# Kernel optimization log

Hardware: AMD Instinct MI355X
Metric: run time of the kernel (lower is better)

## Reference

```python
import jax, jax.numpy as jnp
import numpy as np
from jax import lax

SCORE_THRESHOLD = 0.02
IOU_THRESHOLD = 0.5
NUM_CLASSES = 80
MAX_DETECTIONS = 10  # tf.image.non_max_suppression max_output_size in the source
ANCHORS = np.array([[1.08, 1.19], [3.42, 4.41], [6.63, 11.38], [9.42, 5.11], [16.62, 10.52]], dtype=np.float32)


def setup_inputs() -> dict:
    key = jax.random.key(0)
    k1, _ = jax.random.split(key)
    B, H, W = 16, 76, 76
    A = ANCHORS.shape[0]
    feats = jax.random.normal(k1, (B, H, W, A * (5 + NUM_CLASSES)), dtype=jnp.float32)
    anchors = jnp.asarray(ANCHORS)
    return {"feats": feats, "anchors": anchors}


def yolo_head(feats, anchors, num_classes):
    """Standard YOLOv2 decode (interpret_prediction)."""
    B, H, W, _ = feats.shape
    A = anchors.shape[0]
    feats = feats.reshape(B, H, W, A, 5 + num_classes)
    gy, gx = jnp.meshgrid(jnp.arange(H), jnp.arange(W), indexing="ij")
    grid = jnp.stack([gx, gy], axis=-1).astype(feats.dtype)  # [H,W,2] in (x,y) order
    conv_dims = jnp.array([W, H], dtype=feats.dtype)
    box_xy = (jax.nn.sigmoid(feats[..., 0:2]) + grid[None, :, :, None, :]) / conv_dims
    box_wh = jnp.exp(feats[..., 2:4]) * anchors[None, None, None, :, :] / conv_dims
    box_confidence = jax.nn.sigmoid(feats[..., 4:5])
    box_class_probs = jax.nn.softmax(feats[..., 5:], axis=-1)
    return box_xy, box_wh, box_confidence, box_class_probs


def _postprocess(feats, anchors):
    box_xy, box_wh, box_confidence, box_class_probs = yolo_head(feats, anchors, NUM_CLASSES)
    box_mins = box_xy - box_wh / 2.0
    box_maxes = box_xy + box_wh / 2.0
    # [y_min, x_min, y_max, x_max] as in the source (indices 1 then 0)
    boxes = jnp.concatenate([box_mins[..., 1:2], box_mins[..., 0:1], box_maxes[..., 1:2], box_maxes[..., 0:1]], axis=-1)
    box_scores = box_confidence * box_class_probs           # [B,H,W,A,C]
    box_classes = jnp.argmax(box_scores, axis=-1)           # [B,H,W,A]
    box_class_scores = jnp.max(box_scores, axis=-1)         # [B,H,W,A]

    # tf.boolean_mask flattens across all dims; emulate with fixed shapes by
    # marking below-threshold candidates as invalid (score -1).
    flat_boxes = boxes.reshape(-1, 4)                       # [N,4]
    flat_scores = box_class_scores.reshape(-1)              # [N]
    flat_classes = box_classes.reshape(-1)                  # [N]
    scores_work = jnp.where(flat_scores >= SCORE_THRESHOLD, flat_scores, -1.0)

    N = flat_boxes.shape[0]
    areas = jnp.maximum(flat_boxes[:, 2] - flat_boxes[:, 0], 0.0) * jnp.maximum(flat_boxes[:, 3] - flat_boxes[:, 1], 0.0)
    idx_range = jnp.arange(N)

    def step(sw, _):
        idx = jnp.argmax(sw)
        s = sw[idx]
        valid = s >= SCORE_THRESHOLD
        box = flat_boxes[idx]                               # [4] = y1,x1,y2,x2
        iy1 = jnp.maximum(box[0], flat_boxes[:, 0])
        ix1 = jnp.maximum(box[1], flat_boxes[:, 1])
        iy2 = jnp.minimum(box[2], flat_boxes[:, 2])
        ix2 = jnp.minimum(box[3], flat_boxes[:, 3])
        inter = jnp.maximum(iy2 - iy1, 0.0) * jnp.maximum(ix2 - ix1, 0.0)
        box_area = jnp.maximum(box[2] - box[0], 0.0) * jnp.maximum(box[3] - box[1], 0.0)
        iou = inter / (box_area + areas - inter + 1e-9)
        suppress = (iou > IOU_THRESHOLD) | (idx_range == idx)
        sw_new = jnp.where(valid & suppress, -1.0, sw)
        row = jnp.concatenate([box, s[None], flat_classes[idx].astype(jnp.float32)[None]])  # [6]
        row = jnp.where(valid, row, jnp.zeros_like(row))
        return sw_new, row

    _, rows = lax.scan(step, scores_work, None, length=MAX_DETECTIONS)
    return rows  # [MAX_DETECTIONS, 6] = [y1,x1,y2,x2,score,class]; zero rows are padding


def reference(feats, anchors):
    return _postprocess(feats, anchors)
```

## Files before the change

### kernel.cpp

```cpp
#include <hip/hip_runtime.h>
#include <stdint.h>

#define N_CAND 462080
#define NBINS  8192
#define HIST_BLOCKS 64
#define TARGET 256u
#define SMAX   1024
#define SCORE_THR 0.02f


typedef const __attribute__((address_space(1))) uint32_t* gas1_u32;
typedef __attribute__((address_space(3))) uint32_t*       las3_u32;
#define GLOAD_LDS16(g, l) __builtin_amdgcn_global_load_lds( \
    (gas1_u32)(const void*)(g), (las3_u32)(void*)(l), 16, 0, 0)

__global__ __launch_bounds__(64) void decode_kernel(
    const float* __restrict__ feats,
    float* __restrict__ scores, unsigned char* __restrict__ cls)
{
    __shared__ __align__(16) float lds[64 * 85];
    const int t = threadIdx.x;
    const long long base = (long long)blockIdx.x * 64;

    const float4* __restrict__ src = (const float4*)(feats + base * 85);
    float4* dst = (float4*)lds;
#pragma unroll
    for (int i = 0; i < 21; ++i)
        GLOAD_LDS16(src + i * 64 + t, dst + i * 64 + t);
    if (t < 16) GLOAD_LDS16(src + 21 * 64 + t, dst + 21 * 64 + t);

    asm volatile("s_waitcnt vmcnt(0)" ::: "memory");
    __builtin_amdgcn_sched_barrier(0);

    const float* f = lds + t * 85;
    const int ci = (int)base + t;

    float m = f[5];
    int cbest = 0;
#pragma unroll
    for (int k = 1; k < 80; ++k) {
        float v = f[5 + k];
        if (v > m) { m = v; cbest = k; }
    }
    float s0 = 0.f, s1 = 0.f, s2 = 0.f, s3 = 0.f;
#pragma unroll
    for (int k = 0; k < 80; k += 4) {
        s0 += __expf(f[5 + k] - m);
        s1 += __expf(f[6 + k] - m);
        s2 += __expf(f[7 + k] - m);
        s3 += __expf(f[8 + k] - m);
    }
    float ssum = (s0 + s1) + (s2 + s3);
    float conf = 1.0f / (1.0f + __expf(-f[4]));
    float score = conf * (1.0f / ssum);

    cls[ci] = (unsigned char)cbest;
    scores[ci] = (score >= SCORE_THR) ? score : -1.0f;
}

__global__ __launch_bounds__(1024) void hist_kernel(
    const float* __restrict__ scores, unsigned short* __restrict__ hist_part)
{
    __shared__ unsigned int lh[NBINS];
    const int t = threadIdx.x;
#pragma unroll
    for (int i = 0; i < 8; ++i) lh[t * 8 + i] = 0u;
    __syncthreads();

    for (int i = blockIdx.x * 1024 + t; i < N_CAND; i += HIST_BLOCKS * 1024) {
        float s = scores[i];
        if (s >= SCORE_THR) {
            int bin = (int)(s * (float)NBINS);
            bin = bin > (NBINS - 1) ? (NBINS - 1) : bin;
            atomicAdd(&lh[bin], 1u);
        }
    }
    __syncthreads();
    unsigned short* outp = hist_part + (size_t)blockIdx.x * NBINS;
#pragma unroll
    for (int i = 0; i < 8; ++i)
        outp[t * 8 + i] = (unsigned short)lh[t * 8 + i];
}

__global__ __launch_bounds__(1024) void cutoff_kernel(
    const unsigned short* __restrict__ hist_part, unsigned int* __restrict__ ctrl)
{
    __shared__ unsigned int lh[NBINS];
    __shared__ unsigned int pa[1024], pb[1024];
    const int t = threadIdx.x;

    unsigned bsum[8];
#pragma unroll
    for (int i = 0; i < 8; ++i) bsum[i] = 0u;
    for (int p = 0; p < HIST_BLOCKS; ++p) {
        const unsigned short* hp = hist_part + (size_t)p * NBINS + t * 8;
#pragma unroll
        for (int i = 0; i < 8; ++i) bsum[i] += hp[i];
    }
    unsigned s = 0;
#pragma unroll
    for (int i = 0; i < 8; ++i) { lh[t * 8 + i] = bsum[i]; s += bsum[i]; }
    pa[t] = s;
    __syncthreads();

    unsigned int* srcb = pa; unsigned int* dstb = pb;
    for (int off = 1; off < 1024; off <<= 1) {
        unsigned v = srcb[t] + ((t + off < 1024) ? srcb[t + off] : 0u);
        dstb[t] = v;
        __syncthreads();
        unsigned int* tmp = srcb; srcb = dstb; dstb = tmp;
    }
    unsigned St = srcb[t];
    unsigned Sn = (t < 1023) ? srcb[t + 1] : 0u;

    if (t == 0) {
        ctrl[0] = 0u;
        if (St < TARGET) ctrl[1] = 0u;
    }
    if (St >= TARGET && Sn < TARGET) {
        unsigned run = Sn;
#pragma unroll
        for (int i = 7; i >= 0; --i) {
            run += lh[t * 8 + i];
            if (run >= TARGET) { ctrl[1] = (unsigned)(t * 8 + i); break; }
        }
    }
}

__global__ __launch_bounds__(256) void compact_kernel(
    const float* __restrict__ scores, unsigned int* __restrict__ ctrl,
    float* __restrict__ lscore, int* __restrict__ lidx)
{
    int i = blockIdx.x * 256 + threadIdx.x;
    float sw = scores[i];
    if (sw >= SCORE_THR) {
        int bin = (int)(sw * (float)NBINS);
        bin = bin > (NBINS - 1) ? (NBINS - 1) : bin;
        if (bin >= (int)ctrl[1]) {
            unsigned pos = atomicAdd(&ctrl[0], 1u);
            if (pos < SMAX) { lscore[pos] = sw; lidx[pos] = i; }
        }
    }
}

__device__ inline float4 decode_box(const float* __restrict__ feats,
                                    const float* __restrict__ anchors, int ci)
{
    int a = ci % 5;
    int cell = ci / 5;
    int gx = cell % 76;
    int gy = (cell / 76) % 76;
    const float* f = feats + (long long)ci * 85;
    float bx = (1.0f / (1.0f + __expf(-f[0])) + (float)gx) / 76.0f;
    float by = (1.0f / (1.0f + __expf(-f[1])) + (float)gy) / 76.0f;
    float bw = __expf(f[2]) * anchors[2 * a]     / 76.0f;
    float bh = __expf(f[3]) * anchors[2 * a + 1] / 76.0f;
    return make_float4(by - bh * 0.5f, bx - bw * 0.5f,
                       by + bh * 0.5f, bx + bw * 0.5f);
}

__global__ __launch_bounds__(1024) void nms_kernel(
    const float* __restrict__ lscore, const int* __restrict__ lidx,
    const unsigned int* __restrict__ ctrl,
    const float* __restrict__ feats, const float* __restrict__ anchors,
    const unsigned char* __restrict__ cls, float* __restrict__ out)
{
    __shared__ unsigned long long wkey[16];
    __shared__ unsigned long long bkey;
    __shared__ float4 bbox;
    const int t = threadIdx.x;

    unsigned cnt = ctrl[0];
    int n = (cnt < (unsigned)SMAX) ? (int)cnt : SMAX;

    unsigned long long key = 0ull;
    float4 mb = make_float4(0.f, 0.f, 0.f, 0.f);
    float  msc = 0.f, mcls = 0.f;
    unsigned midx = 0xFFFFFFFFu;
    bool aliveb = false;
    if (t < n) {
        msc  = lscore[t];
        midx = (unsigned)lidx[t];
        key  = ((unsigned long long)__float_as_uint(msc) << 32)
             | (unsigned long long)(0xFFFFFFFFu - midx);
        mb   = decode_box(feats, anchors, (int)midx);
        mcls = (float)cls[midx];
        aliveb = true;
    }

    for (int r = 0; r < 10; ++r) {
        unsigned long long k0 = aliveb ? key : 0ull;
#pragma unroll
        for (int msk = 32; msk > 0; msk >>= 1) {
            unsigned long long o = __shfl_xor(k0, msk);
            k0 = (o > k0) ? o : k0;
        }
        if ((t & 63) == 0) wkey[t >> 6] = k0;
        __syncthreads();
        if (t < 16) {
            unsigned long long v = wkey[t];
#pragma unroll
            for (int msk = 8; msk > 0; msk >>= 1) {
                unsigned long long o = __shfl_xor(v, msk);
                v = (o > v) ? o : v;
            }
            if (t == 0) bkey = v;
        }
        __syncthreads();

        unsigned long long wk = bkey;
        bool have = (wk != 0ull);
        unsigned widx = 0xFFFFFFFFu;
        if (have) widx = 0xFFFFFFFFu - (unsigned)(wk & 0xFFFFFFFFull);

        if (have && aliveb && midx == widx) {
            bbox = mb;
            out[r * 6 + 0] = mb.x;
            out[r * 6 + 1] = mb.y;
            out[r * 6 + 2] = mb.z;
            out[r * 6 + 3] = mb.w;
            out[r * 6 + 4] = msc;
            out[r * 6 + 5] = mcls;
            aliveb = false;
        }
        if (!have && t == 0) {
#pragma unroll
            for (int q = 0; q < 6; ++q) out[r * 6 + q] = 0.f;
        }
        __syncthreads();

        if (have && aliveb) {
            float4 ab = bbox;
            float aarea = fmaxf(ab.z - ab.x, 0.f) * fmaxf(ab.w - ab.y, 0.f);
            float iy1 = fmaxf(ab.x, mb.x);
            float ix1 = fmaxf(ab.y, mb.y);
            float iy2 = fminf(ab.z, mb.z);
            float ix2 = fminf(ab.w, mb.w);
            float inter = fmaxf(iy2 - iy1, 0.f) * fmaxf(ix2 - ix1, 0.f);
            float carea = fmaxf(mb.z - mb.x, 0.f) * fmaxf(mb.w - mb.y, 0.f);
            float iou = inter / (aarea + carea - inter + 1e-9f);
            if (iou > 0.5f) aliveb = false;
        }
    }
}

extern "C" void kernel_launch(void* const* d_in, const int* in_sizes, int n_in,
                              void* d_out, int out_size, void* d_ws, size_t ws_size,
                              hipStream_t stream) {
    const float* feats   = (const float*)d_in[0];
    const float* anchors = (const float*)d_in[1];
    char* ws = (char*)d_ws;

    unsigned int*   ctrl      = (unsigned int*)(ws + 0);
    unsigned short* hist_part = (unsigned short*)(ws + 256);
    float*          lscore    = (float*)(ws + 1048832);
    int*            lidx      = (int*)(ws + 1052928);
    float*          scores    = (float*)(ws + 1057024);
    unsigned char*  cls       = (unsigned char*)(ws + 2905344);
    float*          out       = (float*)d_out;

    decode_kernel <<<N_CAND / 64, 64, 0, stream>>>(feats, scores, cls);
    hist_kernel   <<<HIST_BLOCKS, 1024, 0, stream>>>(scores, hist_part);
    cutoff_kernel <<<1, 1024, 0, stream>>>(hist_part, ctrl);
    compact_kernel<<<N_CAND / 256, 256, 0, stream>>>(scores, ctrl, lscore, lidx);
    nms_kernel    <<<1, 1024, 0, stream>>>(lscore, lidx, ctrl, feats, anchors, cls, out);
}
```

Measured before the change: 65.25 us.

## Fuse cutoff into histogram and NMS into compaction via last-block counters

Merges the single-block cutoff kernel into the histogram kernel and the single-block NMS kernel into the compaction kernel. In each fused kernel, the last block to finish, found with an atomic counter and thread fences, runs the serial stage. The counters are reset inside the decode kernel. This removes two kernel launches and their gaps, and halves the number of histogram partials, at the cost of relying on fence ordering and a tail stage that runs serially in one block.

Measured after the change: 182.0 us. +178.9%, slower.

```diff
diff --git a/kernel.cpp b/kernel.cpp
--- a/kernel.cpp
+++ b/kernel.cpp
@@ -3,10 +3,12 @@
 
 #define N_CAND 462080
 #define NBINS  8192
-#define HIST_BLOCKS 64
+#define HIST_BLOCKS 32
 #define TARGET 256u
 #define SMAX   1024
 #define SCORE_THR 0.02f
+#define CPB 1024
+#define COMPACT_BLOCKS ((N_CAND + CPB - 1) / CPB)
 
 
 typedef const __attribute__((address_space(1))) uint32_t* gas1_u32;
@@ -16,11 +18,14 @@
 
 __global__ __launch_bounds__(64) void decode_kernel(
     const float* __restrict__ feats,
-    float* __restrict__ scores, unsigned char* __restrict__ cls)
+    float* __restrict__ scores, unsigned char* __restrict__ cls,
+    unsigned int* __restrict__ ctrl)
 {
     __shared__ __align__(16) float lds[64 * 85];
     const int t = threadIdx.x;
     const long long base = (long long)blockIdx.x * 64;
+
+    if (blockIdx.x == 0 && t == 0) { ctrl[2] = 0u; ctrl[3] = 0u; }
 
     const float4* __restrict__ src = (const float4*)(feats + base * 85);
     float4* dst = (float4*)lds;
@@ -58,11 +63,15 @@
     scores[ci] = (score >= SCORE_THR) ? score : -1.0f;
 }
 
-__global__ __launch_bounds__(1024) void hist_kernel(
-    const float* __restrict__ scores, unsigned short* __restrict__ hist_part)
+__global__ __launch_bounds__(1024) void hist_cutoff_kernel(
+    const float* __restrict__ scores, unsigned short* __restrict__ hist_part,
+    unsigned int* __restrict__ ctrl)
 {
     __shared__ unsigned int lh[NBINS];
+    __shared__ unsigned int pa[1024], pb[1024];
+    __shared__ int lastf;
     const int t = threadIdx.x;
+
 #pragma unroll
     for (int i = 0; i < 8; ++i) lh[t * 8 + i] = 0u;
     __syncthreads();
@@ -80,14 +89,15 @@
 #pragma unroll
     for (int i = 0; i < 8; ++i)
         outp[t * 8 + i] = (unsigned short)lh[t * 8 + i];
-}
-
-__global__ __launch_bounds__(1024) void cutoff_kernel(
-    const unsigned short* __restrict__ hist_part, unsigned int* __restrict__ ctrl)
-{
-    __shared__ unsigned int lh[NBINS];
-    __shared__ unsigned int pa[1024], pb[1024];
-    const int t = threadIdx.x;
+
+    __threadfence();
+    if (t == 0) {
+        unsigned old = atomicAdd(&ctrl[2], 1u);
+        lastf = (old == HIST_BLOCKS - 1) ? 1 : 0;
+    }
+    __syncthreads();
+    if (!lastf) return;
+    __threadfence();
 
     unsigned bsum[8];
 #pragma unroll
@@ -97,6 +107,7 @@
 #pragma unroll
         for (int i = 0; i < 8; ++i) bsum[i] += hp[i];
     }
+    __syncthreads();
     unsigned s = 0;
 #pragma unroll
     for (int i = 0; i < 8; ++i) { lh[t * 8 + i] = bsum[i]; s += bsum[i]; }
@@ -123,22 +134,6 @@
         for (int i = 7; i >= 0; --i) {
             run += lh[t * 8 + i];
             if (run >= TARGET) { ctrl[1] = (unsigned)(t * 8 + i); break; }
-        }
-    }
-}
-
-__global__ __launch_bounds__(256) void compact_kernel(
-    const float* __restrict__ scores, unsigned int* __restrict__ ctrl,
-    float* __restrict__ lscore, int* __restrict__ lidx)
-{
-    int i = blockIdx.x * 256 + threadIdx.x;
-    float sw = scores[i];
-    if (sw >= SCORE_THR) {
-        int bin = (int)(sw * (float)NBINS);
-        bin = bin > (NBINS - 1) ? (NBINS - 1) : bin;
-        if (bin >= (int)ctrl[1]) {
-            unsigned pos = atomicAdd(&ctrl[0], 1u);
-            if (pos < SMAX) { lscore[pos] = sw; lidx[pos] = i; }
         }
     }
 }
@@ -159,16 +154,39 @@
                        by + bh * 0.5f, bx + bw * 0.5f);
 }
 
-__global__ __launch_bounds__(1024) void nms_kernel(
-    const float* __restrict__ lscore, const int* __restrict__ lidx,
-    const unsigned int* __restrict__ ctrl,
+__global__ __launch_bounds__(1024) void compact_nms_kernel(
+    const float* __restrict__ scores, unsigned int* __restrict__ ctrl,
+    float* __restrict__ lscore, int* __restrict__ lidx,
     const float* __restrict__ feats, const float* __restrict__ anchors,
     const unsigned char* __restrict__ cls, float* __restrict__ out)
 {
     __shared__ unsigned long long wkey[16];
     __shared__ unsigned long long bkey;
     __shared__ float4 bbox;
+    __shared__ int lastf;
     const int t = threadIdx.x;
+    const int i = blockIdx.x * CPB + t;
+
+    if (i < N_CAND) {
+        float sw = scores[i];
+        if (sw >= SCORE_THR) {
+            int bin = (int)(sw * (float)NBINS);
+            bin = bin > (NBINS - 1) ? (NBINS - 1) : bin;
+            if (bin >= (int)ctrl[1]) {
+                unsigned pos = atomicAdd(&ctrl[0], 1u);
+                if (pos < SMAX) { lscore[pos] = sw; lidx[pos] = i; }
+            }
+        }
+    }
+    __syncthreads();
+    __threadfence();
+    if (t == 0) {
+        unsigned old = atomicAdd(&ctrl[3], 1u);
+        lastf = (old == COMPACT_BLOCKS - 1) ? 1 : 0;
+    }
+    __syncthreads();
+    if (!lastf) return;
+    __threadfence();
 
     unsigned cnt = ctrl[0];
     int n = (cnt < (unsigned)SMAX) ? (int)cnt : SMAX;
@@ -210,8 +228,7 @@
 
         unsigned long long wk = bkey;
         bool have = (wk != 0ull);
-        unsigned widx = 0xFFFFFFFFu;
-        if (have) widx = 0xFFFFFFFFu - (unsigned)(wk & 0xFFFFFFFFull);
+        unsigned widx = have ? (0xFFFFFFFFu - (unsigned)(wk & 0xFFFFFFFFull)) : 0xFFFFFFFFu;
 
         if (have && aliveb && midx == widx) {
             bbox = mb;
@@ -253,15 +270,14 @@
 
     unsigned int*   ctrl      = (unsigned int*)(ws + 0);
     unsigned short* hist_part = (unsigned short*)(ws + 256);
-    float*          lscore    = (float*)(ws + 1048832);
-    int*            lidx      = (int*)(ws + 1052928);
-    float*          scores    = (float*)(ws + 1057024);
-    unsigned char*  cls       = (unsigned char*)(ws + 2905344);
+    float*          lscore    = (float*)(ws + 524544);
+    int*            lidx      = (int*)(ws + 528640);
+    float*          scores    = (float*)(ws + 532736);
+    unsigned char*  cls       = (unsigned char*)(ws + 2381056);
     float*          out       = (float*)d_out;
 
-    decode_kernel <<<N_CAND / 64, 64, 0, stream>>>(feats, scores, cls);
-    hist_kernel   <<<HIST_BLOCKS, 1024, 0, stream>>>(scores, hist_part);
-    cutoff_kernel <<<1, 1024, 0, stream>>>(hist_part, ctrl);
-    compact_kernel<<<N_CAND / 256, 256, 0, stream>>>(scores, ctrl, lscore, lidx);
-    nms_kernel    <<<1, 1024, 0, stream>>>(lscore, lidx, ctrl, feats, anchors, cls, out);
-}
+    decode_kernel      <<<N_CAND / 64, 64, 0, stream>>>(feats, scores, cls, ctrl);
+    hist_cutoff_kernel <<<HIST_BLOCKS, 1024, 0, stream>>>(scores, hist_part, ctrl);
+    compact_nms_kernel <<<COMPACT_BLOCKS, 1024, 0, stream>>>(scores, ctrl, lscore, lidx,
+                                                             feats, anchors, cls, out);
+}
```
